# Kernel tuning notes

Measured on AMD Instinct MI355X. Metric: run time of the kernel, lower is better.

## Reference

```python
import jax, jax.numpy as jnp
import numpy as np

B, S_DEC, S_ENC, D, H = 2, 2048, 2048, 1024, 16
HD = D // H  # 64


def setup_inputs() -> dict:
    key = jax.random.key(0)
    ks = jax.random.split(key, 12)
    s = 0.02
    return {
        "dec_hidden_state": jax.random.normal(ks[0], (B, S_DEC, D), jnp.float32),
        "enc_hidden_state": jax.random.normal(ks[1], (B, S_ENC, D), jnp.float32),
        "mask": jnp.ones((B, S_ENC, S_DEC), jnp.int32),
        "Wq": jax.random.normal(ks[2], (H, D, HD), jnp.float32) * s,
        "bq": jax.random.normal(ks[3], (H, HD), jnp.float32) * s,
        "Wk": jax.random.normal(ks[4], (H, D, HD), jnp.float32) * s,
        "bk": jax.random.normal(ks[5], (H, HD), jnp.float32) * s,
        "Wv": jax.random.normal(ks[6], (H, D, HD), jnp.float32) * s,
        "bv": jax.random.normal(ks[7], (H, HD), jnp.float32) * s,
        "Wo": jax.random.normal(ks[8], (D, D), jnp.float32) * s,
        "bo": jax.random.normal(ks[9], (D,), jnp.float32) * s,
    }


def reference(dec_hidden_state, enc_hidden_state, mask, Wq, bq, Wk, bk, Wv, bv, Wo, bo):
    # NOTE: original module swaps args: query <- enc_hidden_state, key/value <- dec_hidden_state.
    # q: [B,H,S_enc,HD], k/v: [B,H,S_dec,HD]
    q = jnp.einsum("bqd,hdk->bhqk", enc_hidden_state, Wq) + bq[None, :, None, :]
    k = jnp.einsum("bsd,hdk->bhsk", dec_hidden_state, Wk) + bk[None, :, None, :]
    v = jnp.einsum("bsd,hdk->bhsk", dec_hidden_state, Wv) + bv[None, :, None, :]
    scores = jnp.einsum("bhqk,bhsk->bhqs", q, k) / jnp.sqrt(jnp.asarray(HD, q.dtype))
    scores = jnp.where(mask[:, None, :, :] == 0, jnp.asarray(-jnp.inf, scores.dtype), scores)
    weights = jax.nn.softmax(scores, axis=-1)
    attn = jnp.einsum("bhqs,bhsk->bhqk", weights, v)  # [B,H,S_enc,HD]
    # concat heads along last dim (same order as torch.cat over head list)
    attn = jnp.transpose(attn, (0, 2, 1, 3)).reshape(B, S_ENC, D)
    return attn @ Wo + bo
```

## Files before the change

### kernel.cpp

```cpp
#include <hip/hip_runtime.h>
#include <math.h>
#include <stdint.h>


typedef unsigned short ushort_t;
typedef __attribute__((ext_vector_type(8))) short short8;
typedef __attribute__((ext_vector_type(4))) float floatx4;

__device__ __forceinline__ ushort_t f2bf(float x){
  unsigned u = __float_as_uint(x);
  u += 0x7fffu + ((u >> 16) & 1u);
  return (ushort_t)(u >> 16);
}
__device__ __forceinline__ unsigned pk2bf(float a, float b){
#if __has_builtin(__builtin_amdgcn_cvt_pk_bf16_f32)
  typedef __attribute__((ext_vector_type(2))) __bf16 bf2_t;
  bf2_t r = __builtin_amdgcn_cvt_pk_bf16_f32(a, b);
  return *(unsigned*)&r;
#else
  return (unsigned)f2bf(a) | ((unsigned)f2bf(b) << 16);
#endif
}
__device__ __forceinline__ floatx4 mfma16(short8 a, short8 b, floatx4 c){
  return __builtin_amdgcn_mfma_f32_16x16x32_bf16(a, b, c, 0, 0, 0);
}
__device__ __forceinline__ void gload16(const void* g, void* l){
  __builtin_amdgcn_global_load_lds((const __attribute__((address_space(1))) void*)g,
                                   (__attribute__((address_space(3))) void*)l, 16, 0, 0);
}

__global__ __launch_bounds__(256)
void prep_kernel(const float* __restrict__ enc, const float* __restrict__ dec,
                 const float* __restrict__ Wq, const float* __restrict__ Wk,
                 const float* __restrict__ Wv, const float* __restrict__ Wo,
                 const int* __restrict__ mask,
                 ushort_t* __restrict__ encb, ushort_t* __restrict__ decb,
                 ushort_t* __restrict__ WqT, ushort_t* __restrict__ WkT,
                 ushort_t* __restrict__ WvT, ushort_t* __restrict__ WoT,
                 unsigned long long* __restrict__ mb)
{
  __shared__ float t[64][65];
  const int bx = blockIdx.x, tid = threadIdx.x;
  if (bx < 8192){
    const float* src = (bx < 4096) ? enc : dec;
    ushort_t*    dst = (bx < 4096) ? encb : decb;
    int i = ((bx & 4095) * 256 + tid) * 4;
    const float4 v = *(const float4*)(src + i);
    unsigned long long p = (unsigned long long)f2bf(v.x)
                         | ((unsigned long long)f2bf(v.y) << 16)
                         | ((unsigned long long)f2bf(v.z) << 32)
                         | ((unsigned long long)f2bf(v.w) << 48);
    *(unsigned long long*)(dst + i) = p;
  } else if (bx < 8960){
    const int id = bx - 8192;
    const int zz = id >> 4, yy = id & 15;
    const int which = zz >> 4, head = zz & 15;
    const float* src = (which == 0) ? Wq : (which == 1) ? Wk : Wv;
    ushort_t*    dst = (which == 0) ? WqT : (which == 1) ? WkT : WvT;
    const long sb = (long)head * 65536;
    const int r0 = yy * 64;
    #pragma unroll
    for (int i = 0; i < 16; i++){
      int idx = i*256 + tid;
      int r = idx >> 6, c = idx & 63;
      t[r][c] = src[sb + (long)(r0 + r)*64 + c];
    }
    __syncthreads();
    #pragma unroll
    for (int i = 0; i < 16; i++){
      int idx = i*256 + tid;
      int cr = idx >> 6, rc = idx & 63;
      dst[sb + (long)cr*1024 + r0 + rc] = f2bf(t[rc][cr]);
    }
  } else if (bx < 9216){
    const int id = bx - 8960;
    const int r0 = (id >> 4) * 64, c0 = (id & 15) * 64;
    #pragma unroll
    for (int i = 0; i < 16; i++){
      int idx = i*256 + tid;
      int r = idx >> 6, c = idx & 63;
      t[r][c] = Wo[(long)(r0 + r)*1024 + c0 + c];
    }
    __syncthreads();
    #pragma unroll
    for (int i = 0; i < 16; i++){
      int idx = i*256 + tid;
      int cr = idx >> 6, rc = idx & 63;
      WoT[(long)(c0 + cr)*1024 + r0 + rc] = f2bf(t[rc][cr]);
    }
  } else {
    long gid = (long)(bx - 9216) * 256 + tid;
    unsigned long long bal = __ballot(mask[gid] != 0);
    if ((tid & 63) == 0) mb[gid >> 6] = bal;
  }
}

__global__ __launch_bounds__(256, 3)
void gemm_qkv_kernel(const ushort_t* __restrict__ encb, const ushort_t* __restrict__ decb,
                     const ushort_t* __restrict__ WqT, const ushort_t* __restrict__ WkT,
                     const ushort_t* __restrict__ WvT,
                     const float* __restrict__ bq, const float* __restrict__ bk,
                     const float* __restrict__ bv,
                     ushort_t* __restrict__ Qb, ushort_t* __restrict__ Kbf,
                     ushort_t* __restrict__ Vtb)
{
  __shared__ ushort_t At[2*4096];
  __shared__ ushort_t Bt[2*4096];
  const int tid = threadIdx.x;
  const int wave = tid >> 6, lane = tid & 63;
  const int quad = lane >> 4, l16 = lane & 15;
  const int z = blockIdx.z;
  const ushort_t *A, *BT; const float* bias; ushort_t* outp;
  int m0, n0; long outAdj = 0;
  float qs = 1.0f;
  if (z == 0){ A = encb; BT = WqT; bias = bq; outp = Qb;  m0 = blockIdx.x*128; n0 = blockIdx.y*128;
               qs = 0.18033688011112042f; }
  else if (z == 1){ A = decb; BT = WkT; bias = bk; outp = Kbf; m0 = blockIdx.x*128; n0 = blockIdx.y*128; }
  else {
    int id = blockIdx.x*8 + blockIdx.y;
    int vb = id >> 7, rem = id & 127;
    m0 = ((rem >> 4) & 7) * 128; n0 = (rem & 15) * 128;
    A = WvT; BT = decb + (long)vb*2097152; bias = bv; outp = Vtb; outAdj = (long)vb*2097152;
  }
  const int K = 1024;

  const int c0 = tid, c1 = 256 + tid;
  const ushort_t* gA0 = A  + (long)(m0 + (c0 >> 2))*K + (c0 & 3)*8;
  const ushort_t* gA1 = A  + (long)(m0 + (c1 >> 2))*K + (c1 & 3)*8;
  const ushort_t* gB0 = BT + (long)(n0 + (c0 >> 2))*K + (c0 & 3)*8;
  const ushort_t* gB1 = BT + (long)(n0 + (c1 >> 2))*K + (c1 & 3)*8;

  floatx4 acc[4][4];
  #pragma unroll
  for (int mt = 0; mt < 4; mt++)
    #pragma unroll
    for (int nt = 0; nt < 4; nt++)
      acc[mt][nt] = (floatx4){0.f, 0.f, 0.f, 0.f};

  short8 rA0 = *(const short8*)gA0;  gA0 += 32;
  short8 rA1 = *(const short8*)gA1;  gA1 += 32;
  short8 rB0 = *(const short8*)gB0;  gB0 += 32;
  short8 rB1 = *(const short8*)gB1;  gB1 += 32;

  const int moff = (wave & 1) * 64, noff = (wave >> 1) * 64;
  int cur = 0;
  for (int k0 = 0; k0 < K; k0 += 32){
    *(short8*)&At[cur*4096 +        tid*8] = rA0;
    *(short8*)&At[cur*4096 + 2048 + tid*8] = rA1;
    *(short8*)&Bt[cur*4096 +        tid*8] = rB0;
    *(short8*)&Bt[cur*4096 + 2048 + tid*8] = rB1;
    __syncthreads();
    if (k0 + 32 < K){
      rA0 = *(const short8*)gA0;  gA0 += 32;
      rA1 = *(const short8*)gA1;  gA1 += 32;
      rB0 = *(const short8*)gB0;  gB0 += 32;
      rB1 = *(const short8*)gB1;  gB1 += 32;
    }
    short8 af[4], bfr[4];
    #pragma unroll
    for (int t = 0; t < 4; t++){
      af[t]  = *(const short8*)&At[cur*4096 + (moff + t*16 + l16)*32 + quad*8];
      bfr[t] = *(const short8*)&Bt[cur*4096 + (noff + t*16 + l16)*32 + quad*8];
    }
    #pragma unroll
    for (int mt = 0; mt < 4; mt++)
      #pragma unroll
      for (int nt = 0; nt < 4; nt++)
        acc[mt][nt] = mfma16(bfr[nt], af[mt], acc[mt][nt]);
    cur ^= 1;
  }

  #pragma unroll
  for (int mt = 0; mt < 4; mt++){
    #pragma unroll
    for (int nt = 0; nt < 4; nt++){
      floatx4 v = acc[mt][nt];
      if (z < 2){
        const int s   = m0 + moff + mt*16 + l16;
        const int ch0 = n0 + noff + nt*16 + quad*4;
        const float4 b4 = *(const float4*)&bias[ch0];
        uint2 pk;
        pk.x = pk2bf((v[0] + b4.x)*qs, (v[1] + b4.y)*qs);
        pk.y = pk2bf((v[2] + b4.z)*qs, (v[3] + b4.w)*qs);
        *(unsigned long long*)&outp[(long)s*1024 + ch0] = *(unsigned long long*)&pk;
      } else {
        const int ch = m0 + moff + mt*16 + l16;
        const int s0 = n0 + noff + nt*16 + quad*4;
        const float bb = bias[ch];
        uint2 pk;
        pk.x = pk2bf(v[0] + bb, v[1] + bb);
        pk.y = pk2bf(v[2] + bb, v[3] + bb);
        *(unsigned long long*)&outp[outAdj + (long)ch*2048 + s0] = *(unsigned long long*)&pk;
      }
    }
  }
}

__global__ __launch_bounds__(256, 2)
void gemm_o_kernel(const ushort_t* __restrict__ A, const ushort_t* __restrict__ BT,
                   const float* __restrict__ bias, float* __restrict__ outf)
{
  __shared__ ushort_t At[2*4096];
  __shared__ ushort_t Bt[2*2048];
  const int tid = threadIdx.x;
  const int wave = tid >> 6, lane = tid & 63;
  const int quad = lane >> 4, l16 = lane & 15;
  const int m0 = blockIdx.x * 128, n0 = blockIdx.y * 64;
  const int K = 1024;

  const int c0 = tid, c1 = 256 + tid;
  const ushort_t* gA0 = A  + (long)(m0 + (c0 >> 2))*K + (c0 & 3)*8;
  const ushort_t* gA1 = A  + (long)(m0 + (c1 >> 2))*K + (c1 & 3)*8;
  const ushort_t* gB0 = BT + (long)(n0 + (c0 >> 2))*K + (c0 & 3)*8;

  floatx4 acc[4][2];
  #pragma unroll
  for (int mt = 0; mt < 4; mt++)
    #pragma unroll
    for (int nt = 0; nt < 2; nt++)
      acc[mt][nt] = (floatx4){0.f, 0.f, 0.f, 0.f};

  short8 rA0 = *(const short8*)gA0;  gA0 += 32;
  short8 rA1 = *(const short8*)gA1;  gA1 += 32;
  short8 rB0 = *(const short8*)gB0;  gB0 += 32;

  const int moff = (wave & 1) * 64, noff = (wave >> 1) * 32;
  int cur = 0;
  for (int k0 = 0; k0 < K; k0 += 32){
    *(short8*)&At[cur*4096 +        tid*8] = rA0;
    *(short8*)&At[cur*4096 + 2048 + tid*8] = rA1;
    *(short8*)&Bt[cur*2048 +        tid*8] = rB0;
    __syncthreads();
    if (k0 + 32 < K){
      rA0 = *(const short8*)gA0;  gA0 += 32;
      rA1 = *(const short8*)gA1;  gA1 += 32;
      rB0 = *(const short8*)gB0;  gB0 += 32;
    }
    short8 af[4], bfr[2];
    #pragma unroll
    for (int t = 0; t < 4; t++)
      af[t]  = *(const short8*)&At[cur*4096 + (moff + t*16 + l16)*32 + quad*8];
    #pragma unroll
    for (int t = 0; t < 2; t++)
      bfr[t] = *(const short8*)&Bt[cur*2048 + (noff + t*16 + l16)*32 + quad*8];
    #pragma unroll
    for (int mt = 0; mt < 4; mt++)
      #pragma unroll
      for (int nt = 0; nt < 2; nt++)
        acc[mt][nt] = mfma16(bfr[nt], af[mt], acc[mt][nt]);
    cur ^= 1;
  }

  #pragma unroll
  for (int mt = 0; mt < 4; mt++){
    #pragma unroll
    for (int nt = 0; nt < 2; nt++){
      const int s   = m0 + moff + mt*16 + l16;
      const int ch0 = n0 + noff + nt*16 + quad*4;
      const float4 b4 = *(const float4*)&bias[ch0];
      float4 o;
      o.x = acc[mt][nt][0] + b4.x;
      o.y = acc[mt][nt][1] + b4.y;
      o.z = acc[mt][nt][2] + b4.z;
      o.w = acc[mt][nt][3] + b4.w;
      *(float4*)&outf[(long)s*1024 + ch0] = o;
    }
  }
}

#define SM_PB(zA_, zB_, wv_, lsum_, pb_)                              \
  {                                                                   \
    float p0 = __builtin_amdgcn_exp2f((zA_)[0]);                      \
    float p1 = __builtin_amdgcn_exp2f((zA_)[1]);                      \
    float p2 = __builtin_amdgcn_exp2f((zA_)[2]);                      \
    float p3 = __builtin_amdgcn_exp2f((zA_)[3]);                      \
    float p4 = __builtin_amdgcn_exp2f((zB_)[0]);                      \
    float p5 = __builtin_amdgcn_exp2f((zB_)[1]);                      \
    float p6 = __builtin_amdgcn_exp2f((zB_)[2]);                      \
    float p7 = __builtin_amdgcn_exp2f((zB_)[3]);                      \
    if (__builtin_expect(!uni, 0)){                                   \
      const int sh_ = quad*8;                                         \
      p0 = (((wv_) >> (sh_+0)) & 1u) ? p0 : 0.f;                      \
      p1 = (((wv_) >> (sh_+1)) & 1u) ? p1 : 0.f;                      \
      p2 = (((wv_) >> (sh_+2)) & 1u) ? p2 : 0.f;                      \
      p3 = (((wv_) >> (sh_+3)) & 1u) ? p3 : 0.f;                      \
      p4 = (((wv_) >> (sh_+4)) & 1u) ? p4 : 0.f;                      \
      p5 = (((wv_) >> (sh_+5)) & 1u) ? p5 : 0.f;                      \
      p6 = (((wv_) >> (sh_+6)) & 1u) ? p6 : 0.f;                      \
      p7 = (((wv_) >> (sh_+7)) & 1u) ? p7 : 0.f;                      \
    }                                                                 \
    lsum_ += ((p0 + p1) + (p2 + p3)) + ((p4 + p5) + (p6 + p7));       \
    unsigned pk0_ = pk2bf(p0, p1);                                    \
    unsigned pk1_ = pk2bf(p2, p3);                                    \
    unsigned pk2_ = pk2bf(p4, p5);                                    \
    unsigned pk3_ = pk2bf(p6, p7);                                    \
    unsigned tmp_[4] = {pk0_, pk1_, pk2_, pk3_};                      \
    __builtin_memcpy(&(pb_), tmp_, 16);                               \
  }

__global__ __launch_bounds__(512, 4)
void flash_attn_kernel(const ushort_t* __restrict__ Qp, const ushort_t* __restrict__ Kp,
                       const ushort_t* __restrict__ Vt, const unsigned* __restrict__ mb,
                       ushort_t* __restrict__ aout)
{
  __shared__ __align__(16) unsigned char smem_raw[65536];
  ushort_t* KBs = (ushort_t*)smem_raw;
  ushort_t* VBs = KBs + 16384;
  float* mO = (float*)smem_raw;
  float* mL = (float*)(smem_raw + 32768);

  const int tid = threadIdx.x, wave = tid >> 6, lane = tid & 63;
  const int quad = lane >> 4, l16 = lane & 15;
  const int shalf = wave >> 2, w = wave & 3;
  const int bh = blockIdx.x, qt = blockIdx.y;
  const int b = bh >> 4, h = bh & 15;

  const ushort_t* VB = Vt + (long)bh*131072;
  const int q0 = qt*128 + w*32;

  const int l8 = lane >> 3, cl = lane & 7;
  const int r0 = w*16 + l8;
  const int sr0 = (r0 & 35) | ((r0 & 4) << 1) | ((r0 & 16) >> 2);
  const int cg = cl ^ l8;
  const ushort_t* kp0 = Kp + ((long)b*2048 + shalf*1024 + sr0)*1024 + h*64 + cg*8;
  const ushort_t* kp1 = kp0 + 16384;
  const ushort_t* vp0 = VB + (long)r0*2048 + shalf*1024 + cg*8;
  const ushort_t* vp1 = vp0 + 16384;
  const int kdo = shalf*16384 + w*2048;
  const int vdo = 32768 + shalf*16384 + w*2048;

  {
    char* kd = (char*)smem_raw + kdo;
    gload16(kp0, kd); gload16(kp1, kd + 1024);
    char* vd = (char*)smem_raw + vdo;
    gload16(vp0, vd); gload16(vp1, vd + 1024);
    kp0 += 65536; kp1 += 65536; vp0 += 64; vp1 += 64;
  }

  short8 qfA0, qfA1, qfB0, qfB1;
  {
    const long qrowA = ((long)b*2048 + q0 + l16)*1024 + h*64;
    qfA0 = *(const short8*)&Qp[qrowA +      quad*8];
    qfA1 = *(const short8*)&Qp[qrowA + 32 + quad*8];
    const long qrowB = qrowA + 16*1024;
    qfB0 = *(const short8*)&Qp[qrowB +      quad*8];
    qfB1 = *(const short8*)&Qp[qrowB + 32 + quad*8];
  }

  floatx4 accA[4], accB[4];
  #pragma unroll
  for (int ht = 0; ht < 4; ht++){
    accA[ht] = (floatx4){0.f,0.f,0.f,0.f};
    accB[ht] = (floatx4){0.f,0.f,0.f,0.f};
  }
  float lsA = 0.f, lsB = 0.f;

  const uint2* mb2 = (const uint2*)mb;
  const long mbase = (long)b*2048 + q0;
  const int sw8 = l16 & 7;
  const int kc0 = (quad ^ sw8) * 8;
  const int kc1 = kc0 ^ 32;

  int cur = 0;
  for (int st = 0; st < 16; st++){
    const uint2 mwA = mb2[(mbase +      l16)*32 + shalf*16 + st];
    const uint2 mwB = mb2[(mbase + 16 + l16)*32 + shalf*16 + st];
    __builtin_amdgcn_sched_barrier(0);
    if (st < 15){
      char* kd = (char*)smem_raw + kdo + (cur^1)*8192;
      gload16(kp0, kd); gload16(kp1, kd + 1024);
      char* vd = (char*)smem_raw + vdo + (cur^1)*8192;
      gload16(vp0, vd); gload16(vp1, vd + 1024);
      kp0 += 65536; kp1 += 65536; vp0 += 64; vp1 += 64;
      asm volatile("s_waitcnt vmcnt(6)" ::: "memory");
    } else {
      asm volatile("s_waitcnt vmcnt(0)" ::: "memory");
    }
    __builtin_amdgcn_s_barrier();
    __builtin_amdgcn_sched_barrier(0);

    const ushort_t* Kt = KBs + shalf*8192 + cur*4096;
    const ushort_t* Vp = VBs + shalf*8192 + cur*4096;
    const bool uni = __all((mwA.x & mwA.y & mwB.x & mwB.y) == 0xFFFFFFFFu);

    #pragma unroll
    for (int c = 0; c < 2; c++){
      const int rA = (c*2    )*16 + l16;
      const int rB = (c*2 + 1)*16 + l16;
      short8 kA0 = *(const short8*)&Kt[rA*64 + kc0];
      short8 kA1 = *(const short8*)&Kt[rA*64 + kc1];
      short8 kB0 = *(const short8*)&Kt[rB*64 + kc0];
      short8 kB1 = *(const short8*)&Kt[rB*64 + kc1];

      floatx4 zA = (floatx4){0.f,0.f,0.f,0.f};
      zA = mfma16(kA0, qfA0, zA);
      zA = mfma16(kA1, qfA1, zA);
      floatx4 zB = (floatx4){0.f,0.f,0.f,0.f};
      zB = mfma16(kB0, qfA0, zB);
      zB = mfma16(kB1, qfA1, zB);
      const unsigned wvA = c ? mwA.y : mwA.x;
      short8 pbA;
      SM_PB(zA, zB, wvA, lsA, pbA);

      zA = (floatx4){0.f,0.f,0.f,0.f};
      zA = mfma16(kA0, qfB0, zA);
      zA = mfma16(kA1, qfB1, zA);
      zB = (floatx4){0.f,0.f,0.f,0.f};
      zB = mfma16(kB0, qfB0, zB);
      zB = mfma16(kB1, qfB1, zB);
      const unsigned wvB = c ? mwB.y : mwB.x;
      short8 pbB;
      SM_PB(zA, zB, wvB, lsB, pbB);

      const int vcs = ((c*4 + quad) ^ sw8) * 8;
      #pragma unroll
      for (int ht = 0; ht < 4; ht++){
        const short8 vf = *(const short8*)&Vp[(ht*16 + l16)*64 + vcs];
        accA[ht] = mfma16(vf, pbA, accA[ht]);
        accB[ht] = mfma16(vf, pbB, accB[ht]);
      }
    }

    asm volatile("s_waitcnt lgkmcnt(0)" ::: "memory");
    __builtin_amdgcn_sched_barrier(0);
    __builtin_amdgcn_s_barrier();
    __builtin_amdgcn_sched_barrier(0);
    cur ^= 1;
  }

  lsA += __shfl_xor(lsA, 16);
  lsA += __shfl_xor(lsA, 32);
  lsB += __shfl_xor(lsB, 16);
  lsB += __shfl_xor(lsB, 32);

  __syncthreads();
  if (shalf == 1){
    #pragma unroll
    for (int ht = 0; ht < 4; ht++){
      *(floatx4*)&mO[((((w*2 + 0)*4 + ht)*64) + lane)*4] = accA[ht];
      *(floatx4*)&mO[((((w*2 + 1)*4 + ht)*64) + lane)*4] = accB[ht];
    }
    mL[(w*2 + 0)*64 + lane] = lsA;
    mL[(w*2 + 1)*64 + lane] = lsB;
  }
  __syncthreads();
  if (shalf == 0){
    const float invA = 1.0f / (lsA + mL[(w*2 + 0)*64 + lane]);
    const float invB = 1.0f / (lsB + mL[(w*2 + 1)*64 + lane]);
    const long rowoA = ((long)b*2048 + q0 + l16)*1024 + h*64;
    const long rowoB = rowoA + 16*1024;
    #pragma unroll
    for (int ht = 0; ht < 4; ht++){
      const floatx4 oA = *(const floatx4*)&mO[((((w*2 + 0)*4 + ht)*64) + lane)*4];
      uint2 pkA;
      pkA.x = pk2bf((accA[ht][0] + oA[0])*invA, (accA[ht][1] + oA[1])*invA);
      pkA.y = pk2bf((accA[ht][2] + oA[2])*invA, (accA[ht][3] + oA[3])*invA);
      *(unsigned long long*)&aout[rowoA + ht*16 + quad*4] = *(unsigned long long*)&pkA;
      const floatx4 oB = *(const floatx4*)&mO[((((w*2 + 1)*4 + ht)*64) + lane)*4];
      uint2 pkB;
      pkB.x = pk2bf((accB[ht][0] + oB[0])*invB, (accB[ht][1] + oB[1])*invB);
      pkB.y = pk2bf((accB[ht][2] + oB[2])*invB, (accB[ht][3] + oB[3])*invB);
      *(unsigned long long*)&aout[rowoB + ht*16 + quad*4] = *(unsigned long long*)&pkB;
    }
  }
}

extern "C" void kernel_launch(void* const* d_in, const int* in_sizes, int n_in,
                              void* d_out, int out_size, void* d_ws, size_t ws_size,
                              hipStream_t stream) {
  const float* dec  = (const float*)d_in[0];
  const float* enc  = (const float*)d_in[1];
  const int*   mask = (const int*)d_in[2];
  const float* Wq   = (const float*)d_in[3];
  const float* bq   = (const float*)d_in[4];
  const float* Wk   = (const float*)d_in[5];
  const float* bk   = (const float*)d_in[6];
  const float* Wv   = (const float*)d_in[7];
  const float* bv   = (const float*)d_in[8];
  const float* Wo   = (const float*)d_in[9];
  const float* bo   = (const float*)d_in[10];
  float* out = (float*)d_out;

  ushort_t* ws   = (ushort_t*)d_ws;
  ushort_t* encb = ws;
  ushort_t* decb = encb + 4194304;
  ushort_t* Qb   = decb + 4194304;
  ushort_t* Kbf  = Qb   + 4194304;
  ushort_t* Vtb  = Kbf  + 4194304;
  ushort_t* WqT  = Vtb  + 4194304;
  ushort_t* WkT  = WqT  + 1048576;
  ushort_t* WvT  = WkT  + 1048576;
  ushort_t* WoT  = WvT  + 1048576;
  unsigned* Mb   = (unsigned*)(WoT + 1048576);

  prep_kernel<<<41984, 256, 0, stream>>>(enc, dec, Wq, Wk, Wv, Wo, mask,
                                         encb, decb, WqT, WkT, WvT, WoT,
                                         (unsigned long long*)Mb);
  gemm_qkv_kernel<<<dim3(32,8,3), 256, 0, stream>>>(encb, decb, WqT, WkT, WvT,
                                                    bq, bk, bv, Qb, Kbf, Vtb);
  flash_attn_kernel<<<dim3(32,16,1), 512, 0, stream>>>(Qb, Kbf, Vtb, Mb, encb);
  gemm_o_kernel<<<dim3(32,16,1), 256, 0, stream>>>(encb, WoT, bo, out);
}
```

Before: 247.0 us.

## Split attention over four key quarters with smaller q tiles and single-buffered LDS

Each attention block now covers 64 queries instead of 128, with 8 waves arranged as 2 query groups by 4 key-sequence quarters. The grid doubles and LDS per block shrinks to about 34 KB, which allows higher occupancy (launch bounds raised to 8). The double-buffered K/V prefetch is replaced by a single-buffered load followed by a full vmcnt(0) wait every step, exposing load latency that more resident blocks must hide. Partial results are combined with a two-stage LDS tree reduction across the four key quarters.

```diff
diff --git a/kernel.cpp b/kernel.cpp
--- a/kernel.cpp
+++ b/kernel.cpp
@@ -298,44 +298,41 @@
     __builtin_memcpy(&(pb_), tmp_, 16);                               \
   }
 
-__global__ __launch_bounds__(512, 4)
+__global__ __launch_bounds__(512, 8)
 void flash_attn_kernel(const ushort_t* __restrict__ Qp, const ushort_t* __restrict__ Kp,
                        const ushort_t* __restrict__ Vt, const unsigned* __restrict__ mb,
                        ushort_t* __restrict__ aout)
 {
-  __shared__ __align__(16) unsigned char smem_raw[65536];
+  __shared__ __align__(16) unsigned char smem_raw[34816];
   ushort_t* KBs = (ushort_t*)smem_raw;
-  ushort_t* VBs = KBs + 16384;
   float* mO = (float*)smem_raw;
   float* mL = (float*)(smem_raw + 32768);
 
   const int tid = threadIdx.x, wave = tid >> 6, lane = tid & 63;
   const int quad = lane >> 4, l16 = lane & 15;
-  const int shalf = wave >> 2, w = wave & 3;
+  const int sq = wave >> 1;
+  const int sp = wave & 1;
+  const int qw = sp;
   const int bh = blockIdx.x, qt = blockIdx.y;
   const int b = bh >> 4, h = bh & 15;
 
   const ushort_t* VB = Vt + (long)bh*131072;
-  const int q0 = qt*128 + w*32;
-
-  const int l8 = lane >> 3, cl = lane & 7;
-  const int r0 = w*16 + l8;
-  const int sr0 = (r0 & 35) | ((r0 & 4) << 1) | ((r0 & 16) >> 2);
-  const int cg = cl ^ l8;
-  const ushort_t* kp0 = Kp + ((long)b*2048 + shalf*1024 + sr0)*1024 + h*64 + cg*8;
-  const ushort_t* kp1 = kp0 + 16384;
-  const ushort_t* vp0 = VB + (long)r0*2048 + shalf*1024 + cg*8;
-  const ushort_t* vp1 = vp0 + 16384;
-  const int kdo = shalf*16384 + w*2048;
-  const int vdo = 32768 + shalf*16384 + w*2048;
-
-  {
-    char* kd = (char*)smem_raw + kdo;
-    gload16(kp0, kd); gload16(kp1, kd + 1024);
-    char* vd = (char*)smem_raw + vdo;
-    gload16(vp0, vd); gload16(vp1, vd + 1024);
-    kp0 += 65536; kp1 += 65536; vp0 += 64; vp1 += 64;
-  }
+  const int q0 = qt*64 + sp*32;
+
+  const int l8 = lane >> 3, cl8 = lane & 7;
+  const int p0r = qw*16 + l8;
+  const int p1r = p0r + 8;
+  const int s0r = ((p0r & 12) << 1) | ((p0r & 16) >> 2) | (p0r & 3);
+  const int s1r = ((p1r & 12) << 1) | ((p1r & 16) >> 2) | (p1r & 3);
+  const int kcg = cl8 ^ l8;
+  const ushort_t* kp0 = Kp + ((long)b*2048 + sq*512 + s0r)*1024 + h*64 + kcg*8;
+  const ushort_t* kp1 = Kp + ((long)b*2048 + sq*512 + s1r)*1024 + h*64 + kcg*8;
+  const int vr0 = qw*32 + (lane >> 2);
+  const int vcg = (lane & 3) ^ ((lane >> 2) & 3) ^ ((lane >> 4) & 3);
+  const ushort_t* vp0 = VB + (long)vr0*2048 + sq*512 + vcg*8;
+  const ushort_t* vp1 = vp0 + 16*2048;
+  char* kd0 = (char*)smem_raw + sq*4096 + qw*2048;
+  char* vd0 = (char*)smem_raw + 16384 + sq*4096 + qw*2048;
 
   short8 qfA0, qfA1, qfB0, qfB1;
   {
@@ -355,77 +352,57 @@
   }
   float lsA = 0.f, lsB = 0.f;
 
-  const uint2* mb2 = (const uint2*)mb;
   const long mbase = (long)b*2048 + q0;
-  const int sw8 = l16 & 7;
-  const int kc0 = (quad ^ sw8) * 8;
+  const int kc0 = (quad ^ (l16 & 7)) * 8;
   const int kc1 = kc0 ^ 32;
-
-  int cur = 0;
+  const int vcs = ((quad ^ (l16 & 3) ^ ((l16 >> 2) & 3)) * 8);
+  const ushort_t* Kt = KBs + sq*2048;
+  const ushort_t* Vp = KBs + 8192 + sq*2048;
+
   for (int st = 0; st < 16; st++){
-    const uint2 mwA = mb2[(mbase +      l16)*32 + shalf*16 + st];
-    const uint2 mwB = mb2[(mbase + 16 + l16)*32 + shalf*16 + st];
-    __builtin_amdgcn_sched_barrier(0);
-    if (st < 15){
-      char* kd = (char*)smem_raw + kdo + (cur^1)*8192;
-      gload16(kp0, kd); gload16(kp1, kd + 1024);
-      char* vd = (char*)smem_raw + vdo + (cur^1)*8192;
-      gload16(vp0, vd); gload16(vp1, vd + 1024);
-      kp0 += 65536; kp1 += 65536; vp0 += 64; vp1 += 64;
-      asm volatile("s_waitcnt vmcnt(6)" ::: "memory");
-    } else {
-      asm volatile("s_waitcnt vmcnt(0)" ::: "memory");
-    }
     __builtin_amdgcn_s_barrier();
     __builtin_amdgcn_sched_barrier(0);
-
-    const ushort_t* Kt = KBs + shalf*8192 + cur*4096;
-    const ushort_t* Vp = VBs + shalf*8192 + cur*4096;
-    const bool uni = __all((mwA.x & mwA.y & mwB.x & mwB.y) == 0xFFFFFFFFu);
-
-    #pragma unroll
-    for (int c = 0; c < 2; c++){
-      const int rA = (c*2    )*16 + l16;
-      const int rB = (c*2 + 1)*16 + l16;
-      short8 kA0 = *(const short8*)&Kt[rA*64 + kc0];
-      short8 kA1 = *(const short8*)&Kt[rA*64 + kc1];
-      short8 kB0 = *(const short8*)&Kt[rB*64 + kc0];
-      short8 kB1 = *(const short8*)&Kt[rB*64 + kc1];
-
-      floatx4 zA = (floatx4){0.f,0.f,0.f,0.f};
-      zA = mfma16(kA0, qfA0, zA);
-      zA = mfma16(kA1, qfA1, zA);
-      floatx4 zB = (floatx4){0.f,0.f,0.f,0.f};
-      zB = mfma16(kB0, qfA0, zB);
-      zB = mfma16(kB1, qfA1, zB);
-      const unsigned wvA = c ? mwA.y : mwA.x;
-      short8 pbA;
-      SM_PB(zA, zB, wvA, lsA, pbA);
-
-      zA = (floatx4){0.f,0.f,0.f,0.f};
-      zA = mfma16(kA0, qfB0, zA);
-      zA = mfma16(kA1, qfB1, zA);
-      zB = (floatx4){0.f,0.f,0.f,0.f};
-      zB = mfma16(kB0, qfB0, zB);
-      zB = mfma16(kB1, qfB1, zB);
-      const unsigned wvB = c ? mwB.y : mwB.x;
-      short8 pbB;
-      SM_PB(zA, zB, wvB, lsB, pbB);
-
-      const int vcs = ((c*4 + quad) ^ sw8) * 8;
-      #pragma unroll
-      for (int ht = 0; ht < 4; ht++){
-        const short8 vf = *(const short8*)&Vp[(ht*16 + l16)*64 + vcs];
-        accA[ht] = mfma16(vf, pbA, accA[ht]);
-        accB[ht] = mfma16(vf, pbB, accB[ht]);
-      }
-    }
-
-    asm volatile("s_waitcnt lgkmcnt(0)" ::: "memory");
+    gload16(kp0, kd0); gload16(kp1, kd0 + 1024);
+    gload16(vp0, vd0); gload16(vp1, vd0 + 1024);
+    kp0 += 32768; kp1 += 32768; vp0 += 32; vp1 += 32;
+    const unsigned mwA = mb[(mbase +      l16)*64 + sq*16 + st];
+    const unsigned mwB = mb[(mbase + 16 + l16)*64 + sq*16 + st];
+    asm volatile("s_waitcnt vmcnt(0)" ::: "memory");
     __builtin_amdgcn_sched_barrier(0);
     __builtin_amdgcn_s_barrier();
     __builtin_amdgcn_sched_barrier(0);
-    cur ^= 1;
+
+    const bool uni = __all((mwA & mwB) == 0xFFFFFFFFu);
+
+    short8 kA0 = *(const short8*)&Kt[(     l16)*64 + kc0];
+    short8 kA1 = *(const short8*)&Kt[(     l16)*64 + kc1];
+    short8 kB0 = *(const short8*)&Kt[(16 + l16)*64 + kc0];
+    short8 kB1 = *(const short8*)&Kt[(16 + l16)*64 + kc1];
+
+    floatx4 zA = (floatx4){0.f,0.f,0.f,0.f};
+    zA = mfma16(kA0, qfA0, zA);
+    zA = mfma16(kA1, qfA1, zA);
+    floatx4 zB = (floatx4){0.f,0.f,0.f,0.f};
+    zB = mfma16(kB0, qfA0, zB);
+    zB = mfma16(kB1, qfA1, zB);
+    short8 pbA;
+    SM_PB(zA, zB, mwA, lsA, pbA);
+
+    zA = (floatx4){0.f,0.f,0.f,0.f};
+    zA = mfma16(kA0, qfB0, zA);
+    zA = mfma16(kA1, qfB1, zA);
+    zB = (floatx4){0.f,0.f,0.f,0.f};
+    zB = mfma16(kB0, qfB0, zB);
+    zB = mfma16(kB1, qfB1, zB);
+    short8 pbB;
+    SM_PB(zA, zB, mwB, lsB, pbB);
+
+    #pragma unroll
+    for (int ht = 0; ht < 4; ht++){
+      const short8 vf = *(const short8*)&Vp[(ht*16 + l16)*32 + vcs];
+      accA[ht] = mfma16(vf, pbA, accA[ht]);
+      accB[ht] = mfma16(vf, pbB, accB[ht]);
+    }
   }
 
   lsA += __shfl_xor(lsA, 16);
@@ -434,32 +411,61 @@
   lsB += __shfl_xor(lsB, 32);
 
   __syncthreads();
-  if (shalf == 1){
+  if (wave >= 4){
+    const int wi = wave - 4;
     #pragma unroll
     for (int ht = 0; ht < 4; ht++){
-      *(floatx4*)&mO[((((w*2 + 0)*4 + ht)*64) + lane)*4] = accA[ht];
-      *(floatx4*)&mO[((((w*2 + 1)*4 + ht)*64) + lane)*4] = accB[ht];
-    }
-    mL[(w*2 + 0)*64 + lane] = lsA;
-    mL[(w*2 + 1)*64 + lane] = lsB;
+      *(floatx4*)&mO[(((wi*2 + 0)*4 + ht)*64 + lane)*4] = accA[ht];
+      *(floatx4*)&mO[(((wi*2 + 1)*4 + ht)*64 + lane)*4] = accB[ht];
+    }
+    mL[(wi*2 + 0)*64 + lane] = lsA;
+    mL[(wi*2 + 1)*64 + lane] = lsB;
   }
   __syncthreads();
-  if (shalf == 0){
-    const float invA = 1.0f / (lsA + mL[(w*2 + 0)*64 + lane]);
-    const float invB = 1.0f / (lsB + mL[(w*2 + 1)*64 + lane]);
+  if (wave < 4){
+    const int wi = wave;
+    #pragma unroll
+    for (int ht = 0; ht < 4; ht++){
+      accA[ht] += *(const floatx4*)&mO[(((wi*2 + 0)*4 + ht)*64 + lane)*4];
+      accB[ht] += *(const floatx4*)&mO[(((wi*2 + 1)*4 + ht)*64 + lane)*4];
+    }
+    lsA += mL[(wi*2 + 0)*64 + lane];
+    lsB += mL[(wi*2 + 1)*64 + lane];
+  }
+  __syncthreads();
+  if (wave == 2 || wave == 3){
+    const int wi = wave - 2;
+    #pragma unroll
+    for (int ht = 0; ht < 4; ht++){
+      *(floatx4*)&mO[(((wi*2 + 0)*4 + ht)*64 + lane)*4] = accA[ht];
+      *(floatx4*)&mO[(((wi*2 + 1)*4 + ht)*64 + lane)*4] = accB[ht];
+    }
+    mL[(wi*2 + 0)*64 + lane] = lsA;
+    mL[(wi*2 + 1)*64 + lane] = lsB;
+  }
+  __syncthreads();
+  if (wave < 2){
+    const int wi = wave;
+    #pragma unroll
+    for (int ht = 0; ht < 4; ht++){
+      accA[ht] += *(const floatx4*)&mO[(((wi*2 + 0)*4 + ht)*64 + lane)*4];
+      accB[ht] += *(const floatx4*)&mO[(((wi*2 + 1)*4 + ht)*64 + lane)*4];
+    }
+    lsA += mL[(wi*2 + 0)*64 + lane];
+    lsB += mL[(wi*2 + 1)*64 + lane];
+    const float invA = 1.0f / lsA;
+    const float invB = 1.0f / lsB;
     const long rowoA = ((long)b*2048 + q0 + l16)*1024 + h*64;
     const long rowoB = rowoA + 16*1024;
     #pragma unroll
     for (int ht = 0; ht < 4; ht++){
-      const floatx4 oA = *(const floatx4*)&mO[((((w*2 + 0)*4 + ht)*64) + lane)*4];
       uint2 pkA;
-      pkA.x = pk2bf((accA[ht][0] + oA[0])*invA, (accA[ht][1] + oA[1])*invA);
-      pkA.y = pk2bf((accA[ht][2] + oA[2])*invA, (accA[ht][3] + oA[3])*invA);
+      pkA.x = pk2bf(accA[ht][0]*invA, accA[ht][1]*invA);
+      pkA.y = pk2bf(accA[ht][2]*invA, accA[ht][3]*invA);
       *(unsigned long long*)&aout[rowoA + ht*16 + quad*4] = *(unsigned long long*)&pkA;
-      const floatx4 oB = *(const floatx4*)&mO[((((w*2 + 1)*4 + ht)*64) + lane)*4];
       uint2 pkB;
-      pkB.x = pk2bf((accB[ht][0] + oB[0])*invB, (accB[ht][1] + oB[1])*invB);
-      pkB.y = pk2bf((accB[ht][2] + oB[2])*invB, (accB[ht][3] + oB[3])*invB);
+      pkB.x = pk2bf(accB[ht][0]*invB, accB[ht][1]*invB);
+      pkB.y = pk2bf(accB[ht][2]*invB, accB[ht][3]*invB);
       *(unsigned long long*)&aout[rowoB + ht*16 + quad*4] = *(unsigned long long*)&pkB;
     }
   }
@@ -498,6 +504,6 @@
                                          (unsigned long long*)Mb);
   gemm_qkv_kernel<<<dim3(32,8,3), 256, 0, stream>>>(encb, decb, WqT, WkT, WvT,
                                                     bq, bk, bv, Qb, Kbf, Vtb);
-  flash_attn_kernel<<<dim3(32,16,1), 512, 0, stream>>>(Qb, Kbf, Vtb, Mb, encb);
+  flash_attn_kernel<<<dim3(32,32,1), 512, 0, stream>>>(Qb, Kbf, Vtb, Mb, encb);
   gemm_o_kernel<<<dim3(32,16,1), 256, 0, stream>>>(encb, WoT, bo, out);
 }
```

Result: slower. 534.7 us (+116.5%).
